# Optimization experiments

Hardware: AMD Instinct MI355X
Metric: run time of the kernel (lower is better)

The kernel has to match this reference:

```python
import jax, jax.numpy as jnp
import numpy as np

# static config (matches init_kwargs)
B = 16
S = 32          # patch grid side
td = 2          # tile_dim
ts = td * td    # tile size
T = (S // td) ** 2
R = 1           # register tokens
U = 1           # tile_comp_size
P = S * S
N = R + P
KC = T * U
K = R + KC
D = 768
H = 12
DH = D // H
HID = 32        # CPB hidden


def setup_inputs() -> dict:
    key = jax.random.key(0)
    ks = jax.random.split(key, 11)
    sc = 0.02
    x = jax.random.normal(ks[0], (B, N, D), jnp.float32)
    logit_w = jax.random.normal(ks[1], (U, D), jnp.float32) * sc
    q_w = jax.random.normal(ks[2], (D, D), jnp.float32) * sc
    kv_w = jax.random.normal(ks[3], (2 * D, D), jnp.float32) * sc
    out_w = jax.random.normal(ks[4], (D, D), jnp.float32) * sc
    out_b = jax.random.normal(ks[5], (D,), jnp.float32) * sc
    cpb_w1 = jax.random.normal(ks[6], (HID, 3), jnp.float32) * 0.5
    cpb_b1 = jax.random.normal(ks[7], (HID,), jnp.float32) * sc
    cpb_w2 = jax.random.normal(ks[8], (H, HID), jnp.float32) * 0.1
    cpb_b2 = jax.random.normal(ks[9], (H,), jnp.float32) * sc
    u_pos = jax.random.normal(ks[10], (1, U, 3), jnp.float32) * sc
    # query patch positions [qx, qy, 0] on the SxS grid (row-major)
    coords = np.arange(S, dtype=np.float32)
    gy, gx = np.meshgrid(coords, coords, indexing='ij')
    P_pos = np.stack([gx.ravel(), gy.ravel(), np.zeros(P, np.float32)], axis=-1)[:, None, :]
    # per-tile centers [cx, cy, 0], tile index t = row_tile*(S//td)+col_tile
    tc = np.arange(S // td, dtype=np.float32) * td + (td - 1) / 2.0
    ty, tx = np.meshgrid(tc, tc, indexing='ij')
    tile_centers = np.stack([tx.ravel(), ty.ravel(), np.zeros(T, np.float32)], axis=-1)[:, None, :]
    return {
        'x': x, 'logit_w': logit_w, 'q_w': q_w, 'kv_w': kv_w,
        'out_w': out_w, 'out_b': out_b,
        'cpb_w1': cpb_w1, 'cpb_b1': cpb_b1, 'cpb_w2': cpb_w2, 'cpb_b2': cpb_b2,
        'u_pos': u_pos,
        'P_pos': jnp.asarray(P_pos), 'tile_centers': jnp.asarray(tile_centers),
    }


def _cpb_bias(P_pos, tile_centers, u_pos, cpb_w1, cpb_b1, cpb_w2, cpb_b2, dtype):
    # anchors: tile center + tied per-U offset -> [KC, 3]
    k_pos = (tile_centers + u_pos).reshape(KC, 3)
    delta = P_pos - k_pos[None, :, :].reshape(1, KC, 3)  # [P, KC, 3]
    dxy, s_feat = delta[..., :2], delta[..., 2:]
    phi_xy = jnp.sign(dxy) * jnp.log1p(jnp.abs(dxy))
    feats = jnp.concatenate([phi_xy, -s_feat], axis=-1)  # [P, KC, 3]
    h = jax.nn.gelu(feats @ cpb_w1.T + cpb_b1, approximate=False)
    out_ctx = h @ cpb_w2.T + cpb_b2  # [P, KC, H]
    bias = jnp.zeros((N, K, H), dtype).at[R:, R:, :].set(out_ctx.astype(dtype))
    return bias.transpose(2, 0, 1)  # [H, N, K]


def reference(x, logit_w, q_w, kv_w, out_w, out_b,
              cpb_w1, cpb_b1, cpb_w2, cpb_b2, u_pos, P_pos, tile_centers):
    Bx = x.shape[0]
    # --- tiled softmax-weighted compression ---
    patch = x[:, R:, :].reshape(Bx, S // td, td, S // td, td, D)
    tiled = patch.transpose(0, 1, 3, 2, 4, 5).reshape(Bx, T, ts, D)  # [B,T,ts,D]
    scores = jnp.einsum('btsd,ud->btsu', tiled, logit_w)             # [B,T,ts,U]
    w = jax.nn.softmax(scores.astype(jnp.float32).transpose(0, 1, 3, 2), axis=-1)
    w = w.astype(scores.dtype)                                       # [B,T,U,ts]
    ctx_learn = jnp.einsum('btus,btsd->btud', w, tiled).reshape(Bx, T * U, D)
    ctx = jnp.concatenate([x[:, :R, :], ctx_learn], axis=1)          # [B,K,D]
    # --- projections ---
    q = jnp.einsum('bnd,ed->bne', x, q_w).reshape(Bx, N, H, DH).transpose(0, 2, 1, 3)
    kv = jnp.einsum('bkd,ed->bke', ctx, kv_w).reshape(Bx, K, 2, H, DH)
    k = kv[:, :, 0].transpose(0, 2, 1, 3)  # [B,H,K,DH]
    v = kv[:, :, 1].transpose(0, 2, 1, 3)
    # --- CPB additive bias + SDPA ---
    bias = _cpb_bias(P_pos, tile_centers, u_pos, cpb_w1, cpb_b1, cpb_w2, cpb_b2, x.dtype)
    scale = DH ** -0.5
    logits = jnp.einsum('bhnd,bhkd->bhnk', q, k) * scale + bias[None]
    attn = jax.nn.softmax(logits, axis=-1)
    o = jnp.einsum('bhnk,bhkd->bhnd', attn, v).transpose(0, 2, 1, 3).reshape(Bx, N, D)
    return o @ out_w.T + out_b
```

## Files before the change

### kernel.cpp

```cpp
#include <hip/hip_runtime.h>
#include <math.h>

namespace {
constexpr int BB   = 16;
constexpr int SS   = 32;
constexpr int TT   = 256;
constexpr int PP   = 1024;
constexpr int NTOK = 1025;
constexpr int KCC  = 256;
constexpr int KTOK = 257;
constexpr int DD   = 768;
constexpr int HH   = 12;
constexpr int DHH  = 64;
constexpr int BNP  = 1040;
}

typedef _Float16 f16x8 __attribute__((ext_vector_type(8)));
typedef _Float16 f16x2 __attribute__((ext_vector_type(2)));
typedef float f32x4 __attribute__((ext_vector_type(4)));

#define GLOAD_LDS16(gsrc, ldst)                                               \
  __builtin_amdgcn_global_load_lds(                                           \
      (const __attribute__((address_space(1))) unsigned int*)(gsrc),          \
      (__attribute__((address_space(3))) unsigned int*)(ldst), 16, 0, 0)

__global__ __launch_bounds__(256) void cvt_weights_kernel(
    const float* __restrict__ q_w, const float* __restrict__ kv_w,
    const float* __restrict__ out_w,
    _Float16* __restrict__ qwh, _Float16* __restrict__ kvwh,
    _Float16* __restrict__ owh) {
  constexpr int NQ = DD * DD;
  constexpr int NK = 2 * DD * DD;
  const int i = (blockIdx.x * 256 + threadIdx.x) * 8;
  const float* src;
  _Float16* dst;
  int off;
  float scale = 1.0f;
  if (i < NQ) { src = q_w; dst = qwh; off = i; scale = 0.125f; }
  else if (i < NQ + NK) { src = kv_w; dst = kvwh; off = i - NQ; }
  else if (i < NQ + NK + NQ) { src = out_w; dst = owh; off = i - NQ - NK; }
  else return;
  const float4 a = *(const float4*)(src + off);
  const float4 b = *(const float4*)(src + off + 4);
  f16x8 o;
  o[0] = (_Float16)(a.x * scale); o[1] = (_Float16)(a.y * scale);
  o[2] = (_Float16)(a.z * scale); o[3] = (_Float16)(a.w * scale);
  o[4] = (_Float16)(b.x * scale); o[5] = (_Float16)(b.y * scale);
  o[6] = (_Float16)(b.z * scale); o[7] = (_Float16)(b.w * scale);
  *(f16x8*)(dst + off) = o;
}

__global__ __launch_bounds__(256) void ctx_kernel(
    const float* __restrict__ x, const float* __restrict__ logit_w,
    _Float16* __restrict__ ctxh, _Float16* __restrict__ xh) {
  const int blk = blockIdx.x;
  const int b = blk >> 8;
  const int t = blk & 255;
  const int tid = threadIdx.x;
  const int lane = tid & 63;
  const int w = tid >> 6;
  const float* xb = x + (size_t)b * NTOK * DD;
  _Float16* xhb = xh + (size_t)b * NTOK * DD;

  int prow[4];
#pragma unroll
  for (int s = 0; s < 4; ++s)
    prow[s] = 1 + ((t >> 4) * 2 + (s >> 1)) * SS + ((t & 15) * 2 + (s & 1));

  float sv[3][4];
  float part[4] = {0.f, 0.f, 0.f, 0.f};
#pragma unroll
  for (int it = 0; it < 3; ++it) {
    const int d = tid + 256 * it;
    const float lw = logit_w[d];
#pragma unroll
    for (int s = 0; s < 4; ++s) {
      const float xv = xb[(size_t)prow[s] * DD + d];
      sv[it][s] = xv;
      part[s] += xv * lw;
      xhb[(size_t)prow[s] * DD + d] = (_Float16)xv;
    }
  }

#pragma unroll
  for (int dd = 1; dd < 64; dd <<= 1)
#pragma unroll
    for (int s = 0; s < 4; ++s) part[s] += __shfl_xor(part[s], dd, 64);
  __shared__ float wred[4][4];
  if (lane == 0)
#pragma unroll
    for (int s = 0; s < 4; ++s) wred[w][s] = part[s];
  __syncthreads();
  float score[4];
#pragma unroll
  for (int s = 0; s < 4; ++s)
    score[s] = wred[0][s] + wred[1][s] + wred[2][s] + wred[3][s];

  const float mx = fmaxf(fmaxf(score[0], score[1]), fmaxf(score[2], score[3]));
  float e[4], sum = 0.f;
#pragma unroll
  for (int s = 0; s < 4; ++s) { e[s] = expf(score[s] - mx); sum += e[s]; }
  const float inv = 1.f / sum;
#pragma unroll
  for (int s = 0; s < 4; ++s) e[s] *= inv;

  _Float16* crow = ctxh + ((size_t)b * KTOK + 1 + t) * DD;
#pragma unroll
  for (int it = 0; it < 3; ++it) {
    const int d = tid + 256 * it;
    float acc = 0.f;
#pragma unroll
    for (int s = 0; s < 4; ++s) acc += e[s] * sv[it][s];
    crow[d] = (_Float16)acc;
  }
  if (t == 0) {
    _Float16* dst = ctxh + (size_t)b * KTOK * DD;
#pragma unroll
    for (int it = 0; it < 3; ++it) {
      const int d = tid + 256 * it;
      const float xv = xb[d];
      dst[d] = (_Float16)xv;
      xhb[d] = (_Float16)xv;
    }
  }
}

template <int OUTF16>
__global__ __launch_bounds__(256) void gemm_f16_kernel(
    const _Float16* __restrict__ A, const _Float16* __restrict__ W,
    const float* __restrict__ bias, void* __restrict__ Cout,
    int M, int Nout, int gx) {
  constexpr int BK = 64;
  __shared__ _Float16 As[128 * BK];
  __shared__ _Float16 Ws[128 * BK];

  const int tid = threadIdx.x;
  const int lane = tid & 63;
  const int w = tid >> 6;
  const int fr = lane & 15;
  const int g = lane >> 4;
  const int awm = (w >> 1) * 64;
  const int awn = (w & 1) * 64;

  const int nwg = gridDim.x;
  const int q8 = nwg >> 3, r8 = nwg & 7;
  const int xcd = blockIdx.x & 7;
  const int base = (xcd < r8) ? xcd * (q8 + 1) : r8 * (q8 + 1) + (xcd - r8) * q8;
  const int wg = base + (blockIdx.x >> 3);
  const int row0 = (wg / gx) * 128;
  const int col0 = (wg % gx) * 128;

  const int srow = lane >> 3;
  const int schunk = (lane & 7) ^ (srow & 7);

  f32x4 acc[4][4];
#pragma unroll
  for (int i = 0; i < 4; ++i)
#pragma unroll
    for (int j = 0; j < 4; ++j) acc[i][j] = (f32x4){0.f, 0.f, 0.f, 0.f};

  for (int k0 = 0; k0 < 768; k0 += BK) {
    __syncthreads();
#pragma unroll
    for (int c = 0; c < 4; ++c) {
      const int rl = w * 32 + c * 8 + srow;
      int ga = row0 + rl;
      ga = ga < M ? ga : M - 1;
      GLOAD_LDS16(A + (size_t)ga * 768 + k0 + schunk * 8, &As[(w * 32 + c * 8) * BK]);
      GLOAD_LDS16(W + (size_t)(col0 + rl) * 768 + k0 + schunk * 8,
                  &Ws[(w * 32 + c * 8) * BK]);
    }
    __syncthreads();

#pragma unroll
    for (int ks = 0; ks < 2; ++ks) {
      f16x8 af[4], bf[4];
#pragma unroll
      for (int i = 0; i < 4; ++i) {
        const int row = awm + i * 16 + fr;
        af[i] = *(const f16x8*)&As[row * BK + (((ks * 4 + g) ^ (fr & 7)) * 8)];
      }
#pragma unroll
      for (int j = 0; j < 4; ++j) {
        const int row = awn + j * 16 + fr;
        bf[j] = *(const f16x8*)&Ws[row * BK + (((ks * 4 + g) ^ (fr & 7)) * 8)];
      }
#pragma unroll
      for (int i = 0; i < 4; ++i)
#pragma unroll
        for (int j = 0; j < 4; ++j)
          acc[i][j] = __builtin_amdgcn_mfma_f32_16x16x32_f16(af[i], bf[j], acc[i][j], 0, 0, 0);
    }
  }

#pragma unroll
  for (int i = 0; i < 4; ++i) {
    const int rbase = row0 + awm + i * 16 + g * 4;
#pragma unroll
    for (int reg = 0; reg < 4; ++reg) {
      const int gr = rbase + reg;
      if (gr >= M) continue;
      if constexpr (OUTF16) {
        _Float16* crow = (_Float16*)Cout + (size_t)gr * Nout + col0;
#pragma unroll
        for (int j = 0; j < 4; ++j)
          crow[awn + j * 16 + fr] = (_Float16)acc[i][j][reg];
      } else {
        float* crow = (float*)Cout + (size_t)gr * Nout + col0;
#pragma unroll
        for (int j = 0; j < 4; ++j) {
          const int gc = awn + j * 16 + fr;
          crow[gc] = acc[i][j][reg] + bias[col0 + gc];
        }
      }
    }
  }
}

__global__ __launch_bounds__(256) void cpb_kernel(
    const float* __restrict__ P_pos, const float* __restrict__ tile_centers,
    const float* __restrict__ u_pos,
    const float* __restrict__ w1, const float* __restrict__ b1,
    const float* __restrict__ w2, const float* __restrict__ b2,
    float* __restrict__ biasK) {
  const int idx = blockIdx.x * 256 + threadIdx.x;
  const int c = idx >> 10;
  const int p = idx & 1023;

  const float px = P_pos[p * 3 + 0], py = P_pos[p * 3 + 1], pz = P_pos[p * 3 + 2];
  const float kx = tile_centers[c * 3 + 0] + u_pos[0];
  const float ky = tile_centers[c * 3 + 1] + u_pos[1];
  const float kz = tile_centers[c * 3 + 2] + u_pos[2];
  const float dx = px - kx, dy = py - ky, dz = pz - kz;
  const float fx = copysignf(log1pf(fabsf(dx)), dx);
  const float fy = copysignf(log1pf(fabsf(dy)), dy);
  const float fz = -dz;

  float outh[HH];
#pragma unroll
  for (int h = 0; h < HH; ++h) outh[h] = b2[h];
  for (int j = 0; j < 32; ++j) {
    float hj = fx * w1[j * 3 + 0] + fy * w1[j * 3 + 1] + fz * w1[j * 3 + 2] + b1[j];
    hj = 0.5f * hj * (1.f + erff(hj * 0.70710678118654752f));
#pragma unroll
    for (int h = 0; h < HH; ++h) outh[h] += hj * w2[h * 32 + j];
  }
#pragma unroll
  for (int h = 0; h < HH; ++h) {
    float* row = biasK + ((size_t)h * KCC + c) * BNP;
    row[1 + p] = outh[h];
    if (p == 0) row[0] = 0.f;
    if (p < BNP - 1 - PP) row[1 + PP + p] = 0.f;
  }
}

__global__ __launch_bounds__(512) void attn_mfma_kernel(
    const _Float16* __restrict__ qf, const _Float16* __restrict__ kvf,
    const float* __restrict__ biasK, _Float16* __restrict__ of) {
  __shared__ _Float16 Kh[4][64 * 64];
  __shared__ _Float16 Vt[4][64 * 64];
  __shared__ _Float16 Pl[8][16 * 64];

  const int tid = threadIdx.x;
  const int lane = tid & 63;
  const int w = tid >> 6;
  const int fr = lane & 15;
  const int g = lane >> 4;

  const int xcd = blockIdx.x & 7;
  const int grp = xcd + 8 * (blockIdx.x >> 3);
  const int b = grp / HH;
  const int h = grp % HH;

  if (tid < 256) {
    const int ksr = tid >> 2;
    const int kc0 = (tid & 3) * 2;
    const int s7 = ksr & 7;
#pragma unroll
    for (int kt = 0; kt < 4; ++kt) {
      const int key = kt * 64 + ksr;
      const _Float16* srcK = kvf + ((size_t)b * KTOK + key) * (2 * DD) + h * DHH;
      *(f16x8*)&Kh[kt][ksr * 64 + ((kc0 ^ s7) * 8)] = *(const f16x8*)(srcK + kc0 * 8);
      *(f16x8*)&Kh[kt][ksr * 64 + (((kc0 + 1) ^ s7) * 8)] = *(const f16x8*)(srcK + kc0 * 8 + 8);
    }
  } else {
    const int t2 = tid - 256;
    const int vkp = t2 & 31;
    const int vdh = (t2 >> 5) * 8;
#pragma unroll
    for (int kt = 0; kt < 4; ++kt) {
      const int kv0 = kt * 64 + 2 * vkp;
      const f16x8 va = *(const f16x8*)(kvf + ((size_t)b * KTOK + kv0) * (2 * DD) + DD + h * DHH + vdh);
      const f16x8 vbv = *(const f16x8*)(kvf + ((size_t)b * KTOK + kv0 + 1) * (2 * DD) + DD + h * DHH + vdh);
#pragma unroll
      for (int e = 0; e < 8; ++e) {
        const int d = vdh + e;
        f16x2 pr; pr[0] = va[e]; pr[1] = vbv[e];
        *(f16x2*)&Vt[kt][d * 64 + (((vkp >> 2) ^ (d & 7)) * 8) + 2 * (vkp & 3)] = pr;
      }
    }
  }

  const _Float16* k256p = kvf + ((size_t)b * KTOK + 256) * (2 * DD) + h * DHH;
  f16x8 kt256[2];
#pragma unroll
  for (int ks = 0; ks < 2; ++ks)
    kt256[ks] = *(const f16x8*)(k256p + ks * 32 + g * 8);
  float v256[4];
#pragma unroll
  for (int j = 0; j < 4; ++j) v256[j] = (float)k256p[DD + j * 16 + fr];

  __syncthreads();

  for (int c = w; c < 65; c += 8) {
    const int qc = c * 16;

    const int qrow = min(qc + fr, NTOK - 1);
    const _Float16* qsrc = qf + ((size_t)b * NTOK + qrow) * DD + h * DHH;
    f16x8 qa[2];
#pragma unroll
    for (int ks = 0; ks < 2; ++ks)
      qa[ks] = *(const f16x8*)(qsrc + ks * 32 + g * 8);

    const int nb = min(qc + g * 4, PP);

    float sp = 0.f;
#pragma unroll
    for (int ks = 0; ks < 2; ++ks)
#pragma unroll
      for (int j = 0; j < 8; ++j)
        sp += (float)qa[ks][j] * (float)kt256[ks][j];
    sp += __shfl_xor(sp, 16, 64);
    sp += __shfl_xor(sp, 32, 64);
    const f32x4 bt = *(const f32x4*)&biasK[((size_t)h * KCC + (KCC - 1)) * BNP + nb];

    float sm[4][4][4];
    __builtin_amdgcn_s_setprio(1);
#pragma unroll
    for (int kt = 0; kt < 4; ++kt) {
#pragma unroll
      for (int f = 0; f < 4; ++f) {
        f32x4 sf = (f32x4){0.f, 0.f, 0.f, 0.f};
#pragma unroll
        for (int ks = 0; ks < 2; ++ks) {
          const f16x8 kf = *(const f16x8*)&Kh[kt][(f * 16 + fr) * 64 + (((ks * 4 + g) ^ (fr & 7)) * 8)];
          sf = __builtin_amdgcn_mfma_f32_16x16x32_f16(qa[ks], kf, sf, 0, 0, 0);
        }
        const int key = kt * 64 + f * 16 + fr;
        const int cl = min(max(key - 1, 0), KCC - 1);
        const f32x4 b4 = *(const f32x4*)&biasK[((size_t)h * KCC + cl) * BNP + nb];
        const float bm = (key >= 1) ? 1.f : 0.f;
#pragma unroll
        for (int r = 0; r < 4; ++r) sm[kt][f][r] = sf[r] + bm * b4[r];
      }
    }
    __builtin_amdgcn_s_setprio(0);

    float lr_[4], p256[4];
#pragma unroll
    for (int r = 0; r < 4; ++r) {
      float m01 = fmaxf(sm[0][0][r], sm[0][1][r]);
      float m23 = fmaxf(sm[0][2][r], sm[0][3][r]);
#pragma unroll
      for (int kt = 1; kt < 4; ++kt) {
        m01 = fmaxf(m01, fmaxf(sm[kt][0][r], sm[kt][1][r]));
        m23 = fmaxf(m23, fmaxf(sm[kt][2][r], sm[kt][3][r]));
      }
      float m = fmaxf(m01, m23);
#pragma unroll
      for (int d = 1; d < 16; d <<= 1) m = fmaxf(m, __shfl_xor(m, d, 64));
      const float s256r = __shfl(sp, g * 4 + r, 64) + bt[r];
      m = fmaxf(m, s256r);

      float rs = 0.f;
#pragma unroll
      for (int kt = 0; kt < 4; ++kt)
#pragma unroll
        for (int f = 0; f < 4; ++f) {
          const float pv = __expf(sm[kt][f][r] - m);
          sm[kt][f][r] = pv;
          rs += pv;
        }
#pragma unroll
      for (int d = 1; d < 16; d <<= 1) rs += __shfl_xor(rs, d, 64);
      p256[r] = __expf(s256r - m);
      lr_[r] = rs + p256[r];
    }

    f32x4 outacc[4];
#pragma unroll
    for (int j = 0; j < 4; ++j) outacc[j] = (f32x4){0.f, 0.f, 0.f, 0.f};

#pragma unroll
    for (int kt = 0; kt < 4; ++kt) {
#pragma unroll
      for (int f = 0; f < 4; ++f)
#pragma unroll
        for (int r = 0; r < 4; ++r) {
          const int prw = g * 4 + r;
          Pl[w][prw * 64 + (((2 * f + (fr >> 3)) ^ (prw & 7)) * 8) + (fr & 7)] =
              (_Float16)sm[kt][f][r];
        }
      __builtin_amdgcn_s_setprio(1);
#pragma unroll
      for (int ks = 0; ks < 2; ++ks) {
        const f16x8 pa = *(const f16x8*)&Pl[w][fr * 64 + (((ks * 4 + g) ^ (fr & 7)) * 8)];
#pragma unroll
        for (int j = 0; j < 4; ++j) {
          const f16x8 vbf = *(const f16x8*)&Vt[kt][(j * 16 + fr) * 64 + (((ks * 4 + g) ^ (fr & 7)) * 8)];
          outacc[j] = __builtin_amdgcn_mfma_f32_16x16x32_f16(pa, vbf, outacc[j], 0, 0, 0);
        }
      }
      __builtin_amdgcn_s_setprio(0);
    }

#pragma unroll
    for (int r = 0; r < 4; ++r) {
      const int n = qc + g * 4 + r;
      if (n >= NTOK) continue;
      const float inv = 1.f / lr_[r];
      _Float16* orow = of + ((size_t)b * NTOK + n) * DD + h * DHH + fr;
#pragma unroll
      for (int j = 0; j < 4; ++j)
        orow[j * 16] = (_Float16)((outacc[j][r] + p256[r] * v256[j]) * inv);
    }
  }
}

extern "C" void kernel_launch(void* const* d_in, const int* in_sizes, int n_in,
                              void* d_out, int out_size, void* d_ws, size_t ws_size,
                              hipStream_t stream) {
  const float* x            = (const float*)d_in[0];
  const float* logit_w      = (const float*)d_in[1];
  const float* q_w          = (const float*)d_in[2];
  const float* kv_w         = (const float*)d_in[3];
  const float* out_w        = (const float*)d_in[4];
  const float* out_b        = (const float*)d_in[5];
  const float* cpb_w1       = (const float*)d_in[6];
  const float* cpb_b1       = (const float*)d_in[7];
  const float* cpb_w2       = (const float*)d_in[8];
  const float* cpb_b2       = (const float*)d_in[9];
  const float* u_pos        = (const float*)d_in[10];
  const float* P_pos        = (const float*)d_in[11];
  const float* tile_centers = (const float*)d_in[12];
  float* out = (float*)d_out;

  const int Mq  = BB * NTOK;
  const int Mkv = BB * KTOK;

  char* p = (char*)d_ws;
  auto alloc = [&](size_t bytes) {
    char* r = p;
    p += (bytes + 255) & ~(size_t)255;
    return r;
  };
  _Float16* xh    = (_Float16*)alloc((size_t)Mq * DD * 2);
  _Float16* ctxh  = (_Float16*)alloc((size_t)Mkv * DD * 2);
  _Float16* qwh   = (_Float16*)alloc((size_t)DD * DD * 2);
  _Float16* kvwh  = (_Float16*)alloc((size_t)2 * DD * DD * 2);
  _Float16* owh   = (_Float16*)alloc((size_t)DD * DD * 2);
  _Float16* qbuf  = (_Float16*)alloc((size_t)Mq * DD * 2);
  _Float16* kvbuf = (_Float16*)alloc((size_t)Mkv * 2 * DD * 2);
  float*    biasK = (float*)alloc((size_t)HH * KCC * BNP * 4);
  _Float16* obuf  = (_Float16*)alloc((size_t)Mq * DD * 2);

  const int n_wt = 4 * DD * DD;

  cvt_weights_kernel<<<(n_wt / 8 + 255) / 256, 256, 0, stream>>>(
      q_w, kv_w, out_w, qwh, kvwh, owh);

  ctx_kernel<<<BB * TT, 256, 0, stream>>>(x, logit_w, ctxh, xh);

  const int gq = 6 * 129;
  const int gk = 12 * 33;
  gemm_f16_kernel<1><<<gq, 256, 0, stream>>>(xh, qwh, nullptr, qbuf, Mq, DD, 6);
  gemm_f16_kernel<1><<<gk, 256, 0, stream>>>(ctxh, kvwh, nullptr, kvbuf, Mkv, 2 * DD, 12);

  cpb_kernel<<<(PP * KCC) / 256, 256, 0, stream>>>(
      P_pos, tile_centers, u_pos, cpb_w1, cpb_b1, cpb_w2, cpb_b2, biasK);

  attn_mfma_kernel<<<BB * HH, 512, 0, stream>>>(qbuf, kvbuf, biasK, obuf);

  gemm_f16_kernel<0><<<gq, 256, 0, stream>>>(obuf, owh, out_b, out, Mq, DD, 6);
}
```

Baseline: 175.4 us.

## Transpose CPB bias to query-major layout and swap MFMA operands in attention

The CPB bias buffer is now laid out per head as [query token][key] with padded rows, zero entries for the register token built in. The attention kernel swaps the MFMA operand order so each lane holds four consecutive keys for a single query row. That lets each lane read its bias as one contiguous f32x4 from that query's row, replacing the strided per-key loads with clamping and masking. Softmax reductions then use two cross-lane shuffles instead of four-step butterflies, and P is written to LDS as packed f16x4 stores. The risk is a larger bias buffer with strided cpb_kernel writes, plus extra shuffles at the output stage to fetch per-row sums.

```diff
diff --git a/kernel.cpp b/kernel.cpp
--- a/kernel.cpp
+++ b/kernel.cpp
@@ -12,10 +12,11 @@
 constexpr int DD   = 768;
 constexpr int HH   = 12;
 constexpr int DHH  = 64;
-constexpr int BNP  = 1040;
+constexpr int BKP  = 272;
 }
 
 typedef _Float16 f16x8 __attribute__((ext_vector_type(8)));
+typedef _Float16 f16x4 __attribute__((ext_vector_type(4)));
 typedef _Float16 f16x2 __attribute__((ext_vector_type(2)));
 typedef float f32x4 __attribute__((ext_vector_type(4)));
 
@@ -222,7 +223,7 @@
     const float* __restrict__ u_pos,
     const float* __restrict__ w1, const float* __restrict__ b1,
     const float* __restrict__ w2, const float* __restrict__ b2,
-    float* __restrict__ biasK) {
+    float* __restrict__ biasT2) {
   const int idx = blockIdx.x * 256 + threadIdx.x;
   const int c = idx >> 10;
   const int p = idx & 1023;
@@ -247,16 +248,21 @@
   }
 #pragma unroll
   for (int h = 0; h < HH; ++h) {
-    float* row = biasK + ((size_t)h * KCC + c) * BNP;
-    row[1 + p] = outh[h];
-    if (p == 0) row[0] = 0.f;
-    if (p < BNP - 1 - PP) row[1 + PP + p] = 0.f;
+    float* base = biasT2 + (size_t)h * NTOK * BKP;
+    base[(size_t)(p + 1) * BKP + (c + 1)] = outh[h];
+    if (c == 0) base[(size_t)(p + 1) * BKP] = 0.f;
+    if (c < BKP - KTOK) base[(size_t)(p + 1) * BKP + KTOK + c] = 0.f;
+    if (p == 0) {
+      base[c + 1] = 0.f;
+      if (c == 0) base[0] = 0.f;
+      if (c < BKP - KTOK) base[KTOK + c] = 0.f;
+    }
   }
 }
 
 __global__ __launch_bounds__(512) void attn_mfma_kernel(
     const _Float16* __restrict__ qf, const _Float16* __restrict__ kvf,
-    const float* __restrict__ biasK, _Float16* __restrict__ of) {
+    const float* __restrict__ biasT2, _Float16* __restrict__ of) {
   __shared__ _Float16 Kh[4][64 * 64];
   __shared__ _Float16 Vt[4][64 * 64];
   __shared__ _Float16 Pl[8][16 * 64];
@@ -322,7 +328,7 @@
     for (int ks = 0; ks < 2; ++ks)
       qa[ks] = *(const f16x8*)(qsrc + ks * 32 + g * 8);
 
-    const int nb = min(qc + g * 4, PP);
+    const float* brow = biasT2 + ((size_t)h * NTOK + qrow) * BKP;
 
     float sp = 0.f;
 #pragma unroll
@@ -332,7 +338,7 @@
         sp += (float)qa[ks][j] * (float)kt256[ks][j];
     sp += __shfl_xor(sp, 16, 64);
     sp += __shfl_xor(sp, 32, 64);
-    const f32x4 bt = *(const f32x4*)&biasK[((size_t)h * KCC + (KCC - 1)) * BNP + nb];
+    const float s256 = sp + brow[256];
 
     float sm[4][4][4];
     __builtin_amdgcn_s_setprio(1);
@@ -343,49 +349,43 @@
         f32x4 sf = (f32x4){0.f, 0.f, 0.f, 0.f};
 #pragma unroll
         for (int ks = 0; ks < 2; ++ks) {
-          const f16x8 kf = *(const f16x8*)&Kh[kt][(f * 16 + fr) * 64 + (((ks * 4 + g) ^ (fr & 7)) * 8)];
-          sf = __builtin_amdgcn_mfma_f32_16x16x32_f16(qa[ks], kf, sf, 0, 0, 0);
+          const f16x8 kfv = *(const f16x8*)&Kh[kt][(f * 16 + fr) * 64 + (((ks * 4 + g) ^ (fr & 7)) * 8)];
+          sf = __builtin_amdgcn_mfma_f32_16x16x32_f16(kfv, qa[ks], sf, 0, 0, 0);
         }
-        const int key = kt * 64 + f * 16 + fr;
-        const int cl = min(max(key - 1, 0), KCC - 1);
-        const f32x4 b4 = *(const f32x4*)&biasK[((size_t)h * KCC + cl) * BNP + nb];
-        const float bm = (key >= 1) ? 1.f : 0.f;
-#pragma unroll
-        for (int r = 0; r < 4; ++r) sm[kt][f][r] = sf[r] + bm * b4[r];
+        const int key0 = kt * 64 + f * 16 + g * 4;
+        const f32x4 b4 = *(const f32x4*)&brow[key0];
+#pragma unroll
+        for (int r = 0; r < 4; ++r) sm[kt][f][r] = sf[r] + b4[r];
       }
     }
     __builtin_amdgcn_s_setprio(0);
 
-    float lr_[4], p256[4];
-#pragma unroll
-    for (int r = 0; r < 4; ++r) {
-      float m01 = fmaxf(sm[0][0][r], sm[0][1][r]);
-      float m23 = fmaxf(sm[0][2][r], sm[0][3][r]);
-#pragma unroll
-      for (int kt = 1; kt < 4; ++kt) {
-        m01 = fmaxf(m01, fmaxf(sm[kt][0][r], sm[kt][1][r]));
-        m23 = fmaxf(m23, fmaxf(sm[kt][2][r], sm[kt][3][r]));
-      }
-      float m = fmaxf(m01, m23);
-#pragma unroll
-      for (int d = 1; d < 16; d <<= 1) m = fmaxf(m, __shfl_xor(m, d, 64));
-      const float s256r = __shfl(sp, g * 4 + r, 64) + bt[r];
-      m = fmaxf(m, s256r);
-
-      float rs = 0.f;
-#pragma unroll
-      for (int kt = 0; kt < 4; ++kt)
-#pragma unroll
-        for (int f = 0; f < 4; ++f) {
+    float m = s256;
+#pragma unroll
+    for (int kt = 0; kt < 4; ++kt)
+#pragma unroll
+      for (int f = 0; f < 4; ++f) {
+        m = fmaxf(m, fmaxf(fmaxf(sm[kt][f][0], sm[kt][f][1]),
+                           fmaxf(sm[kt][f][2], sm[kt][f][3])));
+      }
+    m = fmaxf(m, __shfl_xor(m, 16, 64));
+    m = fmaxf(m, __shfl_xor(m, 32, 64));
+
+    float lv = 0.f;
+#pragma unroll
+    for (int kt = 0; kt < 4; ++kt)
+#pragma unroll
+      for (int f = 0; f < 4; ++f)
+#pragma unroll
+        for (int r = 0; r < 4; ++r) {
           const float pv = __expf(sm[kt][f][r] - m);
           sm[kt][f][r] = pv;
-          rs += pv;
+          lv += pv;
         }
-#pragma unroll
-      for (int d = 1; d < 16; d <<= 1) rs += __shfl_xor(rs, d, 64);
-      p256[r] = __expf(s256r - m);
-      lr_[r] = rs + p256[r];
-    }
+    lv += __shfl_xor(lv, 16, 64);
+    lv += __shfl_xor(lv, 32, 64);
+    const float p256 = __expf(s256 - m);
+    lv += p256;
 
     f32x4 outacc[4];
 #pragma unroll
@@ -394,13 +394,14 @@
 #pragma unroll
     for (int kt = 0; kt < 4; ++kt) {
 #pragma unroll
-      for (int f = 0; f < 4; ++f)
-#pragma unroll
-        for (int r = 0; r < 4; ++r) {
-          const int prw = g * 4 + r;
-          Pl[w][prw * 64 + (((2 * f + (fr >> 3)) ^ (prw & 7)) * 8) + (fr & 7)] =
-              (_Float16)sm[kt][f][r];
-        }
+      for (int f = 0; f < 4; ++f) {
+        f16x4 pk;
+        pk[0] = (_Float16)sm[kt][f][0];
+        pk[1] = (_Float16)sm[kt][f][1];
+        pk[2] = (_Float16)sm[kt][f][2];
+        pk[3] = (_Float16)sm[kt][f][3];
+        *(f16x4*)&Pl[w][fr * 64 + (((2 * f + (g >> 1)) ^ (fr & 7)) * 8) + (g & 1) * 4] = pk;
+      }
       __builtin_amdgcn_s_setprio(1);
 #pragma unroll
       for (int ks = 0; ks < 2; ++ks) {
@@ -418,11 +419,13 @@
     for (int r = 0; r < 4; ++r) {
       const int n = qc + g * 4 + r;
       if (n >= NTOK) continue;
-      const float inv = 1.f / lr_[r];
+      const float lr = __shfl(lv, g * 4 + r, 64);
+      const float pr = __shfl(p256, g * 4 + r, 64);
+      const float inv = 1.f / lr;
       _Float16* orow = of + ((size_t)b * NTOK + n) * DD + h * DHH + fr;
 #pragma unroll
       for (int j = 0; j < 4; ++j)
-        orow[j * 16] = (_Float16)((outacc[j][r] + p256[r] * v256[j]) * inv);
+        orow[j * 16] = (_Float16)((outacc[j][r] + pr * v256[j]) * inv);
     }
   }
 }
@@ -461,7 +464,7 @@
   _Float16* owh   = (_Float16*)alloc((size_t)DD * DD * 2);
   _Float16* qbuf  = (_Float16*)alloc((size_t)Mq * DD * 2);
   _Float16* kvbuf = (_Float16*)alloc((size_t)Mkv * 2 * DD * 2);
-  float*    biasK = (float*)alloc((size_t)HH * KCC * BNP * 4);
+  float*    biasT2= (float*)alloc((size_t)HH * NTOK * BKP * 4);
   _Float16* obuf  = (_Float16*)alloc((size_t)Mq * DD * 2);
 
   const int n_wt = 4 * DD * DD;
@@ -477,9 +480,9 @@
   gemm_f16_kernel<1><<<gk, 256, 0, stream>>>(ctxh, kvwh, nullptr, kvbuf, Mkv, 2 * DD, 12);
 
   cpb_kernel<<<(PP * KCC) / 256, 256, 0, stream>>>(
-      P_pos, tile_centers, u_pos, cpb_w1, cpb_b1, cpb_w2, cpb_b2, biasK);
-
-  attn_mfma_kernel<<<BB * HH, 512, 0, stream>>>(qbuf, kvbuf, biasK, obuf);
+      P_pos, tile_centers, u_pos, cpb_w1, cpb_b1, cpb_w2, cpb_b2, biasT2);
+
+  attn_mfma_kernel<<<BB * HH, 512, 0, stream>>>(qbuf, kvbuf, biasT2, obuf);
 
   gemm_f16_kernel<0><<<gq, 256, 0, stream>>>(obuf, owh, out_b, out, Mq, DD, 6);
 }
```

Result: slower. 293.6 us (+67.4%).
